# Kernel optimization log

Hardware: AMD Instinct MI355X
Metric: run time of the kernel (lower is better)

## Reference

```python
import jax, jax.numpy as jnp
import numpy as np

B, S, D_IN, D_OUT = 8, 2048, 512, 512


def setup_inputs() -> dict:
    key = jax.random.key(0)
    ks = jax.random.split(key, 6)
    return {
        "inputs_for_keys": jax.random.normal(ks[0], (B, S, D_IN), dtype=jnp.float32),
        "inputs_for_values": jax.random.normal(ks[1], (B, S, D_IN), dtype=jnp.float32),
        "inputs_for_queries": jax.random.normal(ks[2], (B, S, D_IN), dtype=jnp.float32),
        "Wq": jax.random.normal(ks[3], (D_IN, D_OUT), dtype=jnp.float32) * 0.05,
        "Wk": jax.random.normal(ks[4], (D_IN, D_OUT), dtype=jnp.float32) * 0.05,
        "Wv": jax.random.normal(ks[5], (D_IN, D_OUT), dtype=jnp.float32) * 0.05,
    }


def reference(inputs_for_keys, inputs_for_values, inputs_for_queries, Wq, Wk, Wv):
    # Projections: [B,S,D_in] @ [D_in,D_out] -> [B,S,D_out]
    Q = inputs_for_queries @ Wq
    K = inputs_for_keys @ Wk
    V = inputs_for_values @ Wv
    d_k = K.shape[-1]
    scale = 1.0 / jnp.sqrt(jnp.float32(d_k))
    # Scores: [B,Sq,Sk]
    scores = jnp.einsum("bqd,bkd->bqk", Q, K) * scale
    # Causal mask: original adds -inf for key positions j > query i (use_mask=True)
    q_idx = jnp.arange(Q.shape[1])[:, None]
    k_idx = jnp.arange(K.shape[1])[None, :]
    scores = jnp.where(k_idx > q_idx, jnp.float32(-jnp.inf), scores)
    attn = jax.nn.softmax(scores, axis=-1)
    return jnp.einsum("bqk,bkd->bqd", attn, V)
```

## Files before the change

kernel.cpp:

```cpp
#include <hip/hip_runtime.h>
#include <hip/hip_bf16.h>

typedef __bf16 bf16;
typedef __bf16 bf16x4 __attribute__((ext_vector_type(4)));
typedef __bf16 bf16x8 __attribute__((ext_vector_type(8)));
typedef float f32x4 __attribute__((ext_vector_type(4)));
typedef float f32x16 __attribute__((ext_vector_type(16)));

#define NB 8
#define NS 2048
#define ND 512

static __device__ __forceinline__ f32x4 mfma16(bf16x8 a, bf16x8 b, f32x4 c) {
  return __builtin_amdgcn_mfma_f32_16x16x32_bf16(a, b, c, 0, 0, 0);
}
static __device__ __forceinline__ f32x16 mfma32(bf16x8 a, bf16x8 b, f32x16 c) {
  return __builtin_amdgcn_mfma_f32_32x32x16_bf16(a, b, c, 0, 0, 0);
}
static __device__ __forceinline__ void async16(const bf16* g, bf16* l) {
  __builtin_amdgcn_global_load_lds((const __attribute__((address_space(1))) void*)g,
                                   (__attribute__((address_space(3))) void*)l, 16, 0, 0);
}

#define BAR_VM8_LG0() do { asm volatile("s_waitcnt vmcnt(8) lgkmcnt(0)" ::: "memory"); \
  __builtin_amdgcn_s_barrier(); __builtin_amdgcn_sched_barrier(0); } while (0)
#define BAR_LG0() do { asm volatile("s_waitcnt lgkmcnt(0)" ::: "memory"); \
  __builtin_amdgcn_s_barrier(); __builtin_amdgcn_sched_barrier(0); } while (0)

__global__ void wconv_kernel(const float* __restrict__ Wq,
                             const float* __restrict__ Wk,
                             const float* __restrict__ Wv,
                             bf16* __restrict__ Wt) {
  __shared__ float buf[64][65];
  const int z = blockIdx.z;
  const float* W = (z == 0) ? Wq : (z == 1) ? Wk : Wv;
  const float scale = (z == 0) ? 0.063763537f : 1.0f;
  const int k0 = blockIdx.x * 64, n0 = blockIdx.y * 64;
  const int t = threadIdx.x;
#pragma unroll
  for (int i = 0; i < 16; ++i) {
    int idx = i * 256 + t;
    int kk = idx >> 6, nn = idx & 63;
    buf[kk][nn] = W[(size_t)(k0 + kk) * 512 + n0 + nn];
  }
  __syncthreads();
#pragma unroll
  for (int i = 0; i < 16; ++i) {
    int idx = i * 256 + t;
    int nn = idx >> 6, kk = idx & 63;
    Wt[(size_t)z * 262144 + (size_t)(n0 + nn) * 512 + k0 + (kk ^ ((nn & 7) << 3))] =
        (bf16)(buf[kk][nn] * scale);
  }
}

__launch_bounds__(256)
__global__ void proj_kernel(const float* __restrict__ Xq,
                            const float* __restrict__ Xk,
                            const float* __restrict__ Xv,
                            const bf16* __restrict__ Wt,
                            bf16* __restrict__ Cq,
                            bf16* __restrict__ Ck,
                            bf16* __restrict__ Cv) {
  __shared__ bf16 As[2][128][72];
  __shared__ bf16 WsL[2][8192];
  const int z = blockIdx.z;
  const float* A = (z == 0) ? Xq : (z == 1) ? Xk : Xv;
  const bf16* Wz = Wt + (size_t)z * 262144;
  bf16* C = (z == 0) ? Cq : (z == 1) ? Ck : Cv;

  const int t = threadIdx.x;
  const int lane = t & 63;
  const int w = t >> 6;
  const int wr = w >> 1, wc = w & 1;
  const int bxr = blockIdx.x;
  const int mt = (bxr & 7) * 16 + (bxr >> 3);
  const int bm = mt * 128;
  const int bn = blockIdx.y * 128;

  f32x4 acc[4][4] = {};

  auto stageA = [&](int kc, int bufi) {
    int r0 = t >> 4, seg = t & 15;
#pragma unroll
    for (int p = 0; p < 8; ++p) {
      int r = p * 16 + r0;
      float4 v = *(const float4*)(A + (size_t)(bm + r) * 512 + kc * 64 + seg * 4);
      bf16x4 o = {(bf16)v.x, (bf16)v.y, (bf16)v.z, (bf16)v.w};
      *(bf16x4*)&As[bufi][r][seg * 4] = o;
    }
  };
  auto stageW = [&](int kc, int bufi) {
    const int n = t >> 3, seg = t & 7;
#pragma unroll
    for (int i = 0; i < 4; ++i)
      async16(Wz + (size_t)(bn + i * 32 + n) * 512 + kc * 64 + seg * 8,
              &WsL[bufi][(i * 32 + n) * 64 + seg * 8]);
  };

  stageW(0, 0);
  stageA(0, 0);
  __syncthreads();
  int buf = 0;
  for (int kc = 0; kc < 8; ++kc) {
    if (kc < 7) { stageW(kc + 1, buf ^ 1); stageA(kc + 1, buf ^ 1); }
    const int arow = lane & 15, kq = (lane >> 4) * 8;
#pragma unroll
    for (int kk = 0; kk < 2; ++kk) {
      bf16x8 af[4], bfr[4];
#pragma unroll
      for (int mi = 0; mi < 4; ++mi)
        af[mi] = *(const bf16x8*)&As[buf][wr * 64 + mi * 16 + arow][kk * 32 + kq];
#pragma unroll
      for (int ni = 0; ni < 4; ++ni) {
        int n = wc * 64 + ni * 16 + arow;
        bfr[ni] = *(const bf16x8*)&WsL[buf][n * 64 + ((kk * 32 + kq) ^ ((n & 7) << 3))];
      }
#pragma unroll
      for (int mi = 0; mi < 4; ++mi)
#pragma unroll
        for (int ni = 0; ni < 4; ++ni)
          acc[mi][ni] = mfma16(af[mi], bfr[ni], acc[mi][ni]);
    }
    __syncthreads();
    buf ^= 1;
  }

  const int row0 = (lane >> 4) * 4, col = lane & 15;
#pragma unroll
  for (int mi = 0; mi < 4; ++mi)
#pragma unroll
    for (int ni = 0; ni < 4; ++ni) {
      int cg = bn + wc * 64 + ni * 16 + col;
#pragma unroll
      for (int j = 0; j < 4; ++j) {
        int rg = bm + wr * 64 + mi * 16 + row0 + j;
        bf16 o = (bf16)acc[mi][ni][j];
        if (z == 0) {
          C[(size_t)rg * ND + cg] = o;
        } else if (z == 1) {
          C[(size_t)rg * ND + (cg ^ ((rg & 7) << 3))] = o;
        } else {
          int bb = rg >> 11, s = rg & 2047;
          int ss = (s & ~63) | ((s & 63) ^ ((cg & 7) << 3));
          C[(size_t)bb * (ND * NS) + (size_t)cg * NS + ss] = o;
        }
      }
    }
}

template<int NSPLIT>
__launch_bounds__(512, 2)
__global__ void attn_kernel(const bf16* __restrict__ Qg,
                            const bf16* __restrict__ Kg,
                            const bf16* __restrict__ Vtg,
                            float* __restrict__ Out,
                            bf16* __restrict__ Pn,
                            float* __restrict__ Mp,
                            float* __restrict__ Lp) {
  __shared__ bf16 Ks[64][512];
  __shared__ bf16 Vts[512][64];
  __shared__ float Ss[64][68];
  __shared__ bf16 Ps[64][72];
  __shared__ float m_lds[64], l_lds[64], r_lds[64];

  const int t = threadIdx.x;
  const int lane = t & 63;
  const int w = t >> 6;
  const int id = blockIdx.x;
  const int b = id & 7;
  const int qt = 31 - ((id >> 3) & 31);
  const int h = (NSPLIT == 2) ? (id >> 8) : 0;
  const int q0 = qt * 64;
  const int sm = w >> 2, sn = (w >> 1) & 1, sk = w & 1;
  const int l31 = lane & 31, lhi = lane >> 5;

  int t_begin, t_end;
  {
    int nt = qt + 1;
    int mid = (nt + 1) >> 1;
    if (NSPLIT == 2) { t_begin = h ? mid : 0; t_end = h ? nt : mid; }
    else { t_begin = 0; t_end = nt; }
  }
  const int pidx = (h * 8 + b) * 32 + qt;

  if (NSPLIT == 2 && t_begin >= t_end) {
    if (t < 64) { Mp[pidx * 64 + t] = -1e30f; Lp[pidx * 64 + t] = 0.0f; }
    return;
  }

  const bf16* Qb = Qg + (size_t)b * NS * ND;
  const bf16* Kb = Kg + (size_t)b * NS * ND;
  const bf16* Vb = Vtg + (size_t)b * ND * NS;

  if (t < 64) { m_lds[t] = -1e30f; l_lds[t] = 0.0f; }

  bf16x8 qf[16];
  {
    const bf16* qrow = Qb + (size_t)(q0 + sm * 32 + l31) * ND + sk * 256 + lhi * 8;
#pragma unroll
    for (int kc = 0; kc < 16; ++kc) qf[kc] = *(const bf16x8*)(qrow + kc * 16);
  }
  f32x16 acc[2][2] = {};

  auto stageK = [&](int k0s) {
#pragma unroll
    for (int i = 0; i < 8; ++i)
      async16(Kb + (size_t)(k0s + w * 8 + i) * ND + lane * 8, &Ks[w * 8 + i][0]);
  };
  auto stageV = [&](int k0s) {
#pragma unroll
    for (int i = 0; i < 8; ++i)
      async16(Vb + (size_t)(w * 64 + i * 8 + (lane >> 3)) * NS + k0s + (lane & 7) * 8,
              &Vts[w * 64 + i * 8][0]);
  };

  stageK(t_begin * 64);
  stageV(t_begin * 64);

  for (int it = t_begin; it < t_end; ++it) {
    const int k0 = it * 64;
    const int nx = (it + 1 < t_end ? it + 1 : it) * 64;
    BAR_VM8_LG0();

    __builtin_amdgcn_s_setprio(1);
    f32x16 sacc = {};
    const int kvr = sn * 32 + l31;
    const int swz = (kvr & 7) << 3;
#pragma unroll
    for (int kc = 0; kc < 16; ++kc) {
      int col = (sk * 256 + kc * 16 + lhi * 8) ^ swz;
      bf16x8 bfrag = *(const bf16x8*)&Ks[kvr][col];
      sacc = mfma32(qf[kc], bfrag, sacc);
    }
    __builtin_amdgcn_s_setprio(0);
    if (sk) {
#pragma unroll
      for (int j = 0; j < 16; ++j) {
        int row = (j & 3) + 8 * (j >> 2) + 4 * lhi;
        Ss[sm * 32 + row][sn * 32 + l31] = sacc[j];
      }
    }
    BAR_LG0();
    stageK(nx);
    if (!sk) {
      const bool mask = (it == qt);
#pragma unroll
      for (int j = 0; j < 16; ++j) {
        int row = (j & 3) + 8 * (j >> 2) + 4 * lhi;
        int q = sm * 32 + row, kvc = sn * 32 + l31;
        float v = sacc[j] + Ss[q][kvc];
        if (mask && (k0 + kvc > q0 + q)) v = -1e30f;
        Ss[q][kvc] = v;
      }
    }
    BAR_LG0();

    {
      const int row = t >> 3, sub = t & 7;
      float4 a = *(const float4*)&Ss[row][sub * 8];
      float4 c = *(const float4*)&Ss[row][sub * 8 + 4];
      float mx = fmaxf(fmaxf(fmaxf(a.x, a.y), fmaxf(a.z, a.w)),
                       fmaxf(fmaxf(c.x, c.y), fmaxf(c.z, c.w)));
#pragma unroll
      for (int d = 1; d < 8; d <<= 1) mx = fmaxf(mx, __shfl_xor(mx, d));
      float m_old = m_lds[row];
      float m_new = fmaxf(m_old, mx);
      float p0 = exp2f(a.x - m_new), p1 = exp2f(a.y - m_new);
      float p2 = exp2f(a.z - m_new), p3 = exp2f(a.w - m_new);
      float p4 = exp2f(c.x - m_new), p5 = exp2f(c.y - m_new);
      float p6 = exp2f(c.z - m_new), p7 = exp2f(c.w - m_new);
      float sum = ((p0 + p1) + (p2 + p3)) + ((p4 + p5) + (p6 + p7));
#pragma unroll
      for (int d = 1; d < 8; d <<= 1) sum += __shfl_xor(sum, d);
      bf16x8 pv = {(bf16)p0, (bf16)p1, (bf16)p2, (bf16)p3,
                   (bf16)p4, (bf16)p5, (bf16)p6, (bf16)p7};
      *(bf16x8*)&Ps[row][sub * 8] = pv;
      if (sub == 0) {
        float rs = exp2f(m_old - m_new);
        r_lds[row] = rs;
        m_lds[row] = m_new;
        l_lds[row] = l_lds[row] * rs + sum;
      }
    }
    BAR_VM8_LG0();

    __builtin_amdgcn_s_setprio(1);
#pragma unroll
    for (int mi = 0; mi < 2; ++mi)
#pragma unroll
      for (int j = 0; j < 16; ++j) {
        int row = mi * 32 + (j & 3) + 8 * (j >> 2) + 4 * lhi;
        float rs = r_lds[row];
        acc[mi][0][j] *= rs;
        acc[mi][1][j] *= rs;
      }
#pragma unroll
    for (int kc = 0; kc < 4; ++kc) {
      const int kv0 = kc * 16 + lhi * 8;
      bf16x8 pa0 = *(const bf16x8*)&Ps[l31][kv0];
      bf16x8 pa1 = *(const bf16x8*)&Ps[32 + l31][kv0];
      bf16x8 vb0, vb1;
      { int d0 = w * 64 + l31;      vb0 = *(const bf16x8*)&Vts[d0][kv0 ^ ((d0 & 7) << 3)]; }
      { int d1 = w * 64 + 32 + l31; vb1 = *(const bf16x8*)&Vts[d1][kv0 ^ ((d1 & 7) << 3)]; }
      acc[0][0] = mfma32(pa0, vb0, acc[0][0]);
      acc[0][1] = mfma32(pa0, vb1, acc[0][1]);
      acc[1][0] = mfma32(pa1, vb0, acc[1][0]);
      acc[1][1] = mfma32(pa1, vb1, acc[1][1]);
    }
    __builtin_amdgcn_s_setprio(0);
    BAR_LG0();
    stageV(nx);
  }

  if (NSPLIT == 2) {
    if (t < 64) { Mp[pidx * 64 + t] = m_lds[t]; Lp[pidx * 64 + t] = l_lds[t]; }
    bf16* Ob = Pn + (size_t)pidx * 64 * ND;
#pragma unroll
    for (int mi = 0; mi < 2; ++mi)
#pragma unroll
      for (int j = 0; j < 16; ++j) {
        int row = mi * 32 + (j & 3) + 8 * (j >> 2) + 4 * lhi;
        float inv = 1.0f / l_lds[row];
#pragma unroll
        for (int ni = 0; ni < 2; ++ni)
          Ob[(size_t)row * ND + w * 64 + ni * 32 + l31] = (bf16)(acc[mi][ni][j] * inv);
      }
  } else {
    float* Ob = Out + (size_t)b * NS * ND;
#pragma unroll
    for (int mi = 0; mi < 2; ++mi)
#pragma unroll
      for (int j = 0; j < 16; ++j) {
        int row = mi * 32 + (j & 3) + 8 * (j >> 2) + 4 * lhi;
        float inv = 1.0f / l_lds[row];
#pragma unroll
        for (int ni = 0; ni < 2; ++ni)
          __builtin_nontemporal_store(acc[mi][ni][j] * inv,
              &Ob[(size_t)(q0 + row) * ND + w * 64 + ni * 32 + l31]);
      }
  }
}

__global__ void combine_kernel(const bf16* __restrict__ Pn,
                               const float* __restrict__ Mp,
                               const float* __restrict__ Lp,
                               float* __restrict__ Out) {
  const int total = NB * NS * ND / 4;
  for (int v = blockIdx.x * 256 + threadIdx.x; v < total; v += gridDim.x * 256) {
    int e = v * 4;
    int d = e & 511;
    int s = (e >> 9) & 2047;
    int bb = e >> 20;
    int qt = s >> 6, r = s & 63;
    int p0 = (bb * 32 + qt) * 64 + r;
    int p1 = ((8 + bb) * 32 + qt) * 64 + r;
    float m0 = Mp[p0], l0 = Lp[p0], m1 = Mp[p1], l1 = Lp[p1];
    float M = fmaxf(m0, m1);
    float w0 = l0 * exp2f(m0 - M), w1 = l1 * exp2f(m1 - M);
    float inv = 1.0f / (w0 + w1);
    bf16x4 o0 = *(const bf16x4*)(Pn + (size_t)p0 * ND + d);
    bf16x4 o1 = *(const bf16x4*)(Pn + (size_t)p1 * ND + d);
    f32x4 o;
    o[0] = (w0 * (float)o0[0] + w1 * (float)o1[0]) * inv;
    o[1] = (w0 * (float)o0[1] + w1 * (float)o1[1]) * inv;
    o[2] = (w0 * (float)o0[2] + w1 * (float)o1[2]) * inv;
    o[3] = (w0 * (float)o0[3] + w1 * (float)o1[3]) * inv;
    __builtin_nontemporal_store(o, (f32x4*)(Out + e));
  }
}

extern "C" void kernel_launch(void* const* d_in, const int* in_sizes, int n_in,
                              void* d_out, int out_size, void* d_ws, size_t ws_size,
                              hipStream_t stream) {
  const float* Xk = (const float*)d_in[0];
  const float* Xv = (const float*)d_in[1];
  const float* Xq = (const float*)d_in[2];
  const float* Wq = (const float*)d_in[3];
  const float* Wk = (const float*)d_in[4];
  const float* Wv = (const float*)d_in[5];
  float* Out = (float*)d_out;

  char* ws = (char*)d_ws;
  bf16* Qb = (bf16*)(ws);
  bf16* Kb = (bf16*)(ws + (size_t)16 * 1024 * 1024);
  bf16* Vt = (bf16*)(ws + (size_t)32 * 1024 * 1024);
  bf16* Wt = (bf16*)(ws + (size_t)48 * 1024 * 1024);
  bf16* Pn = (bf16*)(ws + (size_t)50 * 1024 * 1024);
  float* Mp = (float*)(ws + (size_t)82 * 1024 * 1024);
  float* Lp = (float*)(ws + (size_t)82 * 1024 * 1024 + 131072);
  const bool split = ws_size >= (size_t)83 * 1024 * 1024;

  wconv_kernel<<<dim3(8, 8, 3), 256, 0, stream>>>(Wq, Wk, Wv, Wt);
  proj_kernel<<<dim3(128, 4, 3), 256, 0, stream>>>(Xq, Xk, Xv, Wt, Qb, Kb, Vt);
  if (split) {
    attn_kernel<2><<<512, 512, 0, stream>>>(Qb, Kb, Vt, Out, Pn, Mp, Lp);
    combine_kernel<<<2048, 256, 0, stream>>>(Pn, Mp, Lp, Out);
  } else {
    attn_kernel<1><<<256, 512, 0, stream>>>(Qb, Kb, Vt, Out, Pn, Mp, Lp);
  }
}
```

Before: 165.3 us.

## Load V fragments directly to registers and merge split-K score partials in softmax

V tiles are no longer staged through shared memory. Each wave loads its own transposed-V MFMA fragments straight from global memory into registers, prefetched one iteration ahead, and the V swizzle in the projection epilogue is dropped. Both split-K halves of QK^T now write their partial scores to separate LDS buffers, and the softmax pass sums them and applies the causal mask, which removes one barrier per iteration. This cuts LDS traffic and barriers but uses more registers and depends on global-load latency being hidden. The wait counts in BAR_VM8_LG0 were tuned for the old async staging and may no longer match.

```diff
diff --git a/kernel.cpp b/kernel.cpp
--- a/kernel.cpp
+++ b/kernel.cpp
@@ -141,8 +141,7 @@
           C[(size_t)rg * ND + (cg ^ ((rg & 7) << 3))] = o;
         } else {
           int bb = rg >> 11, s = rg & 2047;
-          int ss = (s & ~63) | ((s & 63) ^ ((cg & 7) << 3));
-          C[(size_t)bb * (ND * NS) + (size_t)cg * NS + ss] = o;
+          C[(size_t)bb * (ND * NS) + (size_t)cg * NS + s] = o;
         }
       }
     }
@@ -158,8 +157,7 @@
                             float* __restrict__ Mp,
                             float* __restrict__ Lp) {
   __shared__ bf16 Ks[64][512];
-  __shared__ bf16 Vts[512][64];
-  __shared__ float Ss[64][68];
+  __shared__ float Ss[2][64][68];
   __shared__ bf16 Ps[64][72];
   __shared__ float m_lds[64], l_lds[64], r_lds[64];
 
@@ -201,21 +199,25 @@
     for (int kc = 0; kc < 16; ++kc) qf[kc] = *(const bf16x8*)(qrow + kc * 16);
   }
   f32x16 acc[2][2] = {};
+  bf16x8 vr[8];
 
   auto stageK = [&](int k0s) {
 #pragma unroll
     for (int i = 0; i < 8; ++i)
       async16(Kb + (size_t)(k0s + w * 8 + i) * ND + lane * 8, &Ks[w * 8 + i][0]);
   };
-  auto stageV = [&](int k0s) {
-#pragma unroll
-    for (int i = 0; i < 8; ++i)
-      async16(Vb + (size_t)(w * 64 + i * 8 + (lane >> 3)) * NS + k0s + (lane & 7) * 8,
-              &Vts[w * 64 + i * 8][0]);
+  auto issueV = [&](int k0s) {
+#pragma unroll
+    for (int kc = 0; kc < 4; ++kc)
+#pragma unroll
+      for (int ni = 0; ni < 2; ++ni) {
+        int d = w * 64 + ni * 32 + l31;
+        vr[kc * 2 + ni] = *(const bf16x8*)(Vb + (size_t)d * NS + k0s + kc * 16 + lhi * 8);
+      }
   };
 
   stageK(t_begin * 64);
-  stageV(t_begin * 64);
+  issueV(t_begin * 64);
 
   for (int it = t_begin; it < t_end; ++it) {
     const int k0 = it * 64;
@@ -233,47 +235,42 @@
       sacc = mfma32(qf[kc], bfrag, sacc);
     }
     __builtin_amdgcn_s_setprio(0);
-    if (sk) {
-#pragma unroll
-      for (int j = 0; j < 16; ++j) {
-        int row = (j & 3) + 8 * (j >> 2) + 4 * lhi;
-        Ss[sm * 32 + row][sn * 32 + l31] = sacc[j];
-      }
+#pragma unroll
+    for (int j = 0; j < 16; ++j) {
+      int row = (j & 3) + 8 * (j >> 2) + 4 * lhi;
+      Ss[sk][sm * 32 + row][sn * 32 + l31] = sacc[j];
     }
     BAR_LG0();
     stageK(nx);
-    if (!sk) {
-      const bool mask = (it == qt);
-#pragma unroll
-      for (int j = 0; j < 16; ++j) {
-        int row = (j & 3) + 8 * (j >> 2) + 4 * lhi;
-        int q = sm * 32 + row, kvc = sn * 32 + l31;
-        float v = sacc[j] + Ss[q][kvc];
-        if (mask && (k0 + kvc > q0 + q)) v = -1e30f;
-        Ss[q][kvc] = v;
-      }
-    }
-    BAR_LG0();
 
     {
       const int row = t >> 3, sub = t & 7;
-      float4 a = *(const float4*)&Ss[row][sub * 8];
-      float4 c = *(const float4*)&Ss[row][sub * 8 + 4];
-      float mx = fmaxf(fmaxf(fmaxf(a.x, a.y), fmaxf(a.z, a.w)),
-                       fmaxf(fmaxf(c.x, c.y), fmaxf(c.z, c.w)));
+      float4 a0 = *(const float4*)&Ss[0][row][sub * 8];
+      float4 a1 = *(const float4*)&Ss[0][row][sub * 8 + 4];
+      float4 b0 = *(const float4*)&Ss[1][row][sub * 8];
+      float4 b1 = *(const float4*)&Ss[1][row][sub * 8 + 4];
+      float v[8];
+      v[0] = a0.x + b0.x; v[1] = a0.y + b0.y; v[2] = a0.z + b0.z; v[3] = a0.w + b0.w;
+      v[4] = a1.x + b1.x; v[5] = a1.y + b1.y; v[6] = a1.z + b1.z; v[7] = a1.w + b1.w;
+      if (it == qt) {
+#pragma unroll
+        for (int e = 0; e < 8; ++e)
+          if (k0 + sub * 8 + e > q0 + row) v[e] = -1e30f;
+      }
+      float mx = fmaxf(fmaxf(fmaxf(v[0], v[1]), fmaxf(v[2], v[3])),
+                       fmaxf(fmaxf(v[4], v[5]), fmaxf(v[6], v[7])));
 #pragma unroll
       for (int d = 1; d < 8; d <<= 1) mx = fmaxf(mx, __shfl_xor(mx, d));
       float m_old = m_lds[row];
       float m_new = fmaxf(m_old, mx);
-      float p0 = exp2f(a.x - m_new), p1 = exp2f(a.y - m_new);
-      float p2 = exp2f(a.z - m_new), p3 = exp2f(a.w - m_new);
-      float p4 = exp2f(c.x - m_new), p5 = exp2f(c.y - m_new);
-      float p6 = exp2f(c.z - m_new), p7 = exp2f(c.w - m_new);
-      float sum = ((p0 + p1) + (p2 + p3)) + ((p4 + p5) + (p6 + p7));
+      float p[8];
+#pragma unroll
+      for (int e = 0; e < 8; ++e) p[e] = exp2f(v[e] - m_new);
+      float sum = ((p[0] + p[1]) + (p[2] + p[3])) + ((p[4] + p[5]) + (p[6] + p[7]));
 #pragma unroll
       for (int d = 1; d < 8; d <<= 1) sum += __shfl_xor(sum, d);
-      bf16x8 pv = {(bf16)p0, (bf16)p1, (bf16)p2, (bf16)p3,
-                   (bf16)p4, (bf16)p5, (bf16)p6, (bf16)p7};
+      bf16x8 pv = {(bf16)p[0], (bf16)p[1], (bf16)p[2], (bf16)p[3],
+                   (bf16)p[4], (bf16)p[5], (bf16)p[6], (bf16)p[7]};
       *(bf16x8*)&Ps[row][sub * 8] = pv;
       if (sub == 0) {
         float rs = exp2f(m_old - m_new);
@@ -299,17 +296,13 @@
       const int kv0 = kc * 16 + lhi * 8;
       bf16x8 pa0 = *(const bf16x8*)&Ps[l31][kv0];
       bf16x8 pa1 = *(const bf16x8*)&Ps[32 + l31][kv0];
-      bf16x8 vb0, vb1;
-      { int d0 = w * 64 + l31;      vb0 = *(const bf16x8*)&Vts[d0][kv0 ^ ((d0 & 7) << 3)]; }
-      { int d1 = w * 64 + 32 + l31; vb1 = *(const bf16x8*)&Vts[d1][kv0 ^ ((d1 & 7) << 3)]; }
-      acc[0][0] = mfma32(pa0, vb0, acc[0][0]);
-      acc[0][1] = mfma32(pa0, vb1, acc[0][1]);
-      acc[1][0] = mfma32(pa1, vb0, acc[1][0]);
-      acc[1][1] = mfma32(pa1, vb1, acc[1][1]);
+      acc[0][0] = mfma32(pa0, vr[kc * 2 + 0], acc[0][0]);
+      acc[0][1] = mfma32(pa0, vr[kc * 2 + 1], acc[0][1]);
+      acc[1][0] = mfma32(pa1, vr[kc * 2 + 0], acc[1][0]);
+      acc[1][1] = mfma32(pa1, vr[kc * 2 + 1], acc[1][1]);
     }
     __builtin_amdgcn_s_setprio(0);
-    BAR_LG0();
-    stageV(nx);
+    issueV(nx);
   }
 
   if (NSPLIT == 2) {
```

Result: slower. 176.8 us (+7.0%).

## Restructure attention to 32-wide KV tiles, 256 threads, in-register softmax

Applied to the files above, without the earlier changes.

Rewrites the attention kernel to use 32-key tiles with 256-thread blocks. Each wave keeps its own running max and sum in registers, and the cross-wave score exchange goes through bf16 LDS instead of fp32. The KV split now divides each q-tile's 32-wide key tiles evenly between two blocks, which balances the causal work. The non-split fallback is removed and the V-transpose swizzle is changed to match the new 32-wide layout. The aim is less LDS traffic, fewer barriers and better balance. The trade-off is more iterations, a larger per-wave accumulator (8 f32x16) that raises register pressure, and reduced precision in the partial scores.

```diff
diff --git a/kernel.cpp b/kernel.cpp
--- a/kernel.cpp
+++ b/kernel.cpp
@@ -141,204 +141,183 @@
           C[(size_t)rg * ND + (cg ^ ((rg & 7) << 3))] = o;
         } else {
           int bb = rg >> 11, s = rg & 2047;
-          int ss = (s & ~63) | ((s & 63) ^ ((cg & 7) << 3));
+          int ss = (s & ~31) | ((((s >> 3) & 3) ^ ((cg ^ (cg >> 2)) & 3)) << 3) | (s & 7);
           C[(size_t)bb * (ND * NS) + (size_t)cg * NS + ss] = o;
         }
       }
     }
 }
 
-template<int NSPLIT>
-__launch_bounds__(512, 2)
+__launch_bounds__(256, 2)
 __global__ void attn_kernel(const bf16* __restrict__ Qg,
                             const bf16* __restrict__ Kg,
                             const bf16* __restrict__ Vtg,
-                            float* __restrict__ Out,
                             bf16* __restrict__ Pn,
                             float* __restrict__ Mp,
                             float* __restrict__ Lp) {
-  __shared__ bf16 Ks[64][512];
-  __shared__ bf16 Vts[512][64];
-  __shared__ float Ss[64][68];
-  __shared__ bf16 Ps[64][72];
-  __shared__ float m_lds[64], l_lds[64], r_lds[64];
+  __shared__ bf16 Ks[32 * 512];
+  __shared__ bf16 Vts[512 * 32];
+  __shared__ bf16 Sx[64 * 40];
+  __shared__ bf16 Ps[64 * 40];
+  __shared__ float r_lds[64], l_lds[64];
 
   const int t = threadIdx.x;
   const int lane = t & 63;
   const int w = t >> 6;
+  const int l31 = lane & 31, lhi = lane >> 5;
+  const int sq = w >> 1, sk = w & 1;
   const int id = blockIdx.x;
-  const int b = id & 7;
-  const int qt = 31 - ((id >> 3) & 31);
-  const int h = (NSPLIT == 2) ? (id >> 8) : 0;
+  int b, qt, h;
+  if (id < 256) { b = id & 7; qt = 31 - (id >> 3); h = 0; }
+  else { int j = id - 256; b = j & 7; qt = j >> 3; h = 1; }
   const int q0 = qt * 64;
-  const int sm = w >> 2, sn = (w >> 1) & 1, sk = w & 1;
-  const int l31 = lane & 31, lhi = lane >> 5;
-
-  int t_begin, t_end;
-  {
-    int nt = qt + 1;
-    int mid = (nt + 1) >> 1;
-    if (NSPLIT == 2) { t_begin = h ? mid : 0; t_end = h ? nt : mid; }
-    else { t_begin = 0; t_end = nt; }
-  }
+  const int t_begin = h ? (qt + 1) : 0;
+  const int t_end = h ? (2 * qt + 2) : (qt + 1);
   const int pidx = (h * 8 + b) * 32 + qt;
-
-  if (NSPLIT == 2 && t_begin >= t_end) {
-    if (t < 64) { Mp[pidx * 64 + t] = -1e30f; Lp[pidx * 64 + t] = 0.0f; }
-    return;
-  }
 
   const bf16* Qb = Qg + (size_t)b * NS * ND;
   const bf16* Kb = Kg + (size_t)b * NS * ND;
   const bf16* Vb = Vtg + (size_t)b * ND * NS;
 
-  if (t < 64) { m_lds[t] = -1e30f; l_lds[t] = 0.0f; }
+  const int qg = q0 + sq * 32 + l31;
+  const int qsw = (qg >> 3) & 3;
+  const int ql = sq * 32 + l31;
 
   bf16x8 qf[16];
   {
-    const bf16* qrow = Qb + (size_t)(q0 + sm * 32 + l31) * ND + sk * 256 + lhi * 8;
+    const bf16* qrow = Qb + (size_t)qg * ND + sk * 256 + lhi * 8;
 #pragma unroll
     for (int kc = 0; kc < 16; ++kc) qf[kc] = *(const bf16x8*)(qrow + kc * 16);
   }
-  f32x16 acc[2][2] = {};
+  f32x16 acc[8] = {};
+  float m_run = -1e30f, l_run = 0.0f;
 
   auto stageK = [&](int k0s) {
 #pragma unroll
     for (int i = 0; i < 8; ++i)
-      async16(Kb + (size_t)(k0s + w * 8 + i) * ND + lane * 8, &Ks[w * 8 + i][0]);
+      async16(Kb + (size_t)(k0s + w * 8 + i) * ND + lane * 8, &Ks[(w * 8 + i) * 512]);
   };
   auto stageV = [&](int k0s) {
 #pragma unroll
-    for (int i = 0; i < 8; ++i)
-      async16(Vb + (size_t)(w * 64 + i * 8 + (lane >> 3)) * NS + k0s + (lane & 7) * 8,
-              &Vts[w * 64 + i * 8][0]);
+    for (int i = 0; i < 8; ++i) {
+      int d = (w * 8 + i) * 16 + (lane >> 2);
+      async16(Vb + (size_t)d * NS + k0s + (lane & 3) * 8, &Vts[(w * 8 + i) * 512]);
+    }
   };
 
-  stageK(t_begin * 64);
-  stageV(t_begin * 64);
+  stageK(t_begin * 32);
+  stageV(t_begin * 32);
 
   for (int it = t_begin; it < t_end; ++it) {
-    const int k0 = it * 64;
-    const int nx = (it + 1 < t_end ? it + 1 : it) * 64;
+    const int k0 = it * 32;
+    const int nx = (it + 1 < t_end ? it + 1 : it) * 32;
     BAR_VM8_LG0();
 
     __builtin_amdgcn_s_setprio(1);
     f32x16 sacc = {};
-    const int kvr = sn * 32 + l31;
-    const int swz = (kvr & 7) << 3;
 #pragma unroll
     for (int kc = 0; kc < 16; ++kc) {
-      int col = (sk * 256 + kc * 16 + lhi * 8) ^ swz;
-      bf16x8 bfrag = *(const bf16x8*)&Ks[kvr][col];
-      sacc = mfma32(qf[kc], bfrag, sacc);
+      int col = (sk * 256 + kc * 16 + lhi * 8) ^ ((l31 & 7) << 3);
+      bf16x8 kf = *(const bf16x8*)&Ks[l31 * 512 + col];
+      sacc = mfma32(kf, qf[kc], sacc);
     }
     __builtin_amdgcn_s_setprio(0);
     if (sk) {
 #pragma unroll
-      for (int j = 0; j < 16; ++j) {
-        int row = (j & 3) + 8 * (j >> 2) + 4 * lhi;
-        Ss[sm * 32 + row][sn * 32 + l31] = sacc[j];
+      for (int jg = 0; jg < 4; ++jg) {
+        bf16x4 v = {(bf16)sacc[jg * 4], (bf16)sacc[jg * 4 + 1],
+                    (bf16)sacc[jg * 4 + 2], (bf16)sacc[jg * 4 + 3]};
+        *(bf16x4*)&Sx[ql * 40 + ((jg ^ qsw) << 3) + 4 * lhi] = v;
       }
     }
     BAR_LG0();
     stageK(nx);
+
     if (!sk) {
-      const bool mask = (it == qt);
-#pragma unroll
-      for (int j = 0; j < 16; ++j) {
-        int row = (j & 3) + 8 * (j >> 2) + 4 * lhi;
-        int q = sm * 32 + row, kvc = sn * 32 + l31;
-        float v = sacc[j] + Ss[q][kvc];
-        if (mask && (k0 + kvc > q0 + q)) v = -1e30f;
-        Ss[q][kvc] = v;
-      }
-    }
-    BAR_LG0();
-
-    {
-      const int row = t >> 3, sub = t & 7;
-      float4 a = *(const float4*)&Ss[row][sub * 8];
-      float4 c = *(const float4*)&Ss[row][sub * 8 + 4];
-      float mx = fmaxf(fmaxf(fmaxf(a.x, a.y), fmaxf(a.z, a.w)),
-                       fmaxf(fmaxf(c.x, c.y), fmaxf(c.z, c.w)));
-#pragma unroll
-      for (int d = 1; d < 8; d <<= 1) mx = fmaxf(mx, __shfl_xor(mx, d));
-      float m_old = m_lds[row];
-      float m_new = fmaxf(m_old, mx);
-      float p0 = exp2f(a.x - m_new), p1 = exp2f(a.y - m_new);
-      float p2 = exp2f(a.z - m_new), p3 = exp2f(a.w - m_new);
-      float p4 = exp2f(c.x - m_new), p5 = exp2f(c.y - m_new);
-      float p6 = exp2f(c.z - m_new), p7 = exp2f(c.w - m_new);
-      float sum = ((p0 + p1) + (p2 + p3)) + ((p4 + p5) + (p6 + p7));
-#pragma unroll
-      for (int d = 1; d < 8; d <<= 1) sum += __shfl_xor(sum, d);
-      bf16x8 pv = {(bf16)p0, (bf16)p1, (bf16)p2, (bf16)p3,
-                   (bf16)p4, (bf16)p5, (bf16)p6, (bf16)p7};
-      *(bf16x8*)&Ps[row][sub * 8] = pv;
-      if (sub == 0) {
-        float rs = exp2f(m_old - m_new);
-        r_lds[row] = rs;
-        m_lds[row] = m_new;
-        l_lds[row] = l_lds[row] * rs + sum;
+      float v[16];
+#pragma unroll
+      for (int jg = 0; jg < 4; ++jg) {
+        bf16x4 x = *(const bf16x4*)&Sx[ql * 40 + ((jg ^ qsw) << 3) + 4 * lhi];
+#pragma unroll
+        for (int e = 0; e < 4; ++e) v[jg * 4 + e] = sacc[jg * 4 + e] + (float)x[e];
+      }
+      if (k0 + 31 > q0) {
+#pragma unroll
+        for (int jg = 0; jg < 4; ++jg)
+#pragma unroll
+          for (int e = 0; e < 4; ++e)
+            if (k0 + jg * 8 + 4 * lhi + e > qg) v[jg * 4 + e] = -1e30f;
+      }
+      float mx = v[0];
+#pragma unroll
+      for (int j = 1; j < 16; ++j) mx = fmaxf(mx, v[j]);
+      mx = fmaxf(mx, __shfl_xor(mx, 32));
+      float mn = fmaxf(m_run, mx);
+      float rr = exp2f(m_run - mn);
+      float p[16], sum = 0.0f;
+#pragma unroll
+      for (int j = 0; j < 16; ++j) { p[j] = exp2f(v[j] - mn); sum += p[j]; }
+      sum += __shfl_xor(sum, 32);
+      m_run = mn;
+      l_run = l_run * rr + sum;
+      r_lds[ql] = rr;
+#pragma unroll
+      for (int jg = 0; jg < 4; ++jg) {
+        bf16x4 pv = {(bf16)p[jg * 4], (bf16)p[jg * 4 + 1],
+                     (bf16)p[jg * 4 + 2], (bf16)p[jg * 4 + 3]};
+        *(bf16x4*)&Ps[ql * 40 + ((jg ^ qsw) << 3) + 4 * lhi] = pv;
       }
     }
     BAR_VM8_LG0();
 
+    float rf[16];
+#pragma unroll
+    for (int j = 0; j < 16; ++j)
+      rf[j] = r_lds[sq * 32 + (j & 3) + 8 * (j >> 2) + 4 * lhi];
+#pragma unroll
+    for (int dt = 0; dt < 8; ++dt)
+#pragma unroll
+      for (int j = 0; j < 16; ++j) acc[dt][j] *= rf[j];
+    bf16x8 paf[2];
+#pragma unroll
+    for (int kc = 0; kc < 2; ++kc)
+      paf[kc] = *(const bf16x8*)&Ps[ql * 40 + (((kc * 2 + lhi) ^ qsw) << 3)];
     __builtin_amdgcn_s_setprio(1);
 #pragma unroll
-    for (int mi = 0; mi < 2; ++mi)
-#pragma unroll
-      for (int j = 0; j < 16; ++j) {
-        int row = mi * 32 + (j & 3) + 8 * (j >> 2) + 4 * lhi;
-        float rs = r_lds[row];
-        acc[mi][0][j] *= rs;
-        acc[mi][1][j] *= rs;
-      }
-#pragma unroll
-    for (int kc = 0; kc < 4; ++kc) {
-      const int kv0 = kc * 16 + lhi * 8;
-      bf16x8 pa0 = *(const bf16x8*)&Ps[l31][kv0];
-      bf16x8 pa1 = *(const bf16x8*)&Ps[32 + l31][kv0];
-      bf16x8 vb0, vb1;
-      { int d0 = w * 64 + l31;      vb0 = *(const bf16x8*)&Vts[d0][kv0 ^ ((d0 & 7) << 3)]; }
-      { int d1 = w * 64 + 32 + l31; vb1 = *(const bf16x8*)&Vts[d1][kv0 ^ ((d1 & 7) << 3)]; }
-      acc[0][0] = mfma32(pa0, vb0, acc[0][0]);
-      acc[0][1] = mfma32(pa0, vb1, acc[0][1]);
-      acc[1][0] = mfma32(pa1, vb0, acc[1][0]);
-      acc[1][1] = mfma32(pa1, vb1, acc[1][1]);
+    for (int dt = 0; dt < 8; ++dt) {
+      int d = sk * 256 + dt * 32 + l31;
+      int so = (d ^ (d >> 2)) & 3;
+#pragma unroll
+      for (int kc = 0; kc < 2; ++kc) {
+        bf16x8 vf = *(const bf16x8*)&Vts[d * 32 + (((kc * 2 + lhi) ^ so) << 3)];
+        acc[dt] = mfma32(paf[kc], vf, acc[dt]);
+      }
     }
     __builtin_amdgcn_s_setprio(0);
     BAR_LG0();
     stageV(nx);
   }
 
-  if (NSPLIT == 2) {
-    if (t < 64) { Mp[pidx * 64 + t] = m_lds[t]; Lp[pidx * 64 + t] = l_lds[t]; }
-    bf16* Ob = Pn + (size_t)pidx * 64 * ND;
-#pragma unroll
-    for (int mi = 0; mi < 2; ++mi)
-#pragma unroll
-      for (int j = 0; j < 16; ++j) {
-        int row = mi * 32 + (j & 3) + 8 * (j >> 2) + 4 * lhi;
-        float inv = 1.0f / l_lds[row];
-#pragma unroll
-        for (int ni = 0; ni < 2; ++ni)
-          Ob[(size_t)row * ND + w * 64 + ni * 32 + l31] = (bf16)(acc[mi][ni][j] * inv);
-      }
-  } else {
-    float* Ob = Out + (size_t)b * NS * ND;
-#pragma unroll
-    for (int mi = 0; mi < 2; ++mi)
-#pragma unroll
-      for (int j = 0; j < 16; ++j) {
-        int row = mi * 32 + (j & 3) + 8 * (j >> 2) + 4 * lhi;
-        float inv = 1.0f / l_lds[row];
-#pragma unroll
-        for (int ni = 0; ni < 2; ++ni)
-          __builtin_nontemporal_store(acc[mi][ni][j] * inv,
-              &Ob[(size_t)(q0 + row) * ND + w * 64 + ni * 32 + l31]);
-      }
-  }
+  if (!sk) {
+    l_lds[ql] = l_run;
+    Mp[pidx * 64 + ql] = m_run;
+    Lp[pidx * 64 + ql] = l_run;
+  }
+  __syncthreads();
+  float linv[16];
+#pragma unroll
+  for (int j = 0; j < 16; ++j) {
+    float lv = l_lds[sq * 32 + (j & 3) + 8 * (j >> 2) + 4 * lhi];
+    linv[j] = (lv > 0.0f) ? 1.0f / lv : 0.0f;
+  }
+  bf16* Ob = Pn + (size_t)pidx * 64 * ND;
+#pragma unroll
+  for (int dt = 0; dt < 8; ++dt)
+#pragma unroll
+    for (int j = 0; j < 16; ++j) {
+      int row = sq * 32 + (j & 3) + 8 * (j >> 2) + 4 * lhi;
+      Ob[(size_t)row * ND + sk * 256 + dt * 32 + l31] = (bf16)(acc[dt][j] * linv[j]);
+    }
 }
 
 __global__ void combine_kernel(const bf16* __restrict__ Pn,
@@ -388,14 +367,9 @@
   bf16* Pn = (bf16*)(ws + (size_t)50 * 1024 * 1024);
   float* Mp = (float*)(ws + (size_t)82 * 1024 * 1024);
   float* Lp = (float*)(ws + (size_t)82 * 1024 * 1024 + 131072);
-  const bool split = ws_size >= (size_t)83 * 1024 * 1024;
 
   wconv_kernel<<<dim3(8, 8, 3), 256, 0, stream>>>(Wq, Wk, Wv, Wt);
   proj_kernel<<<dim3(128, 4, 3), 256, 0, stream>>>(Xq, Xk, Xv, Wt, Qb, Kb, Vt);
-  if (split) {
-    attn_kernel<2><<<512, 512, 0, stream>>>(Qb, Kb, Vt, Out, Pn, Mp, Lp);
-    combine_kernel<<<2048, 256, 0, stream>>>(Pn, Mp, Lp, Out);
-  } else {
-    attn_kernel<1><<<256, 512, 0, stream>>>(Qb, Kb, Vt, Out, Pn, Mp, Lp);
-  }
-}
+  attn_kernel<<<512, 256, 0, stream>>>(Qb, Kb, Vt, Pn, Mp, Lp);
+  combine_kernel<<<2048, 256, 0, stream>>>(Pn, Mp, Lp, Out);
+}
```

Measured after the change: 242.9 us. 46.9% more time.

## Pair long and short causal split halves in one persistent attention block

Applied to the files above, without the earlier changes.

Replaces the 512-block split-KV launch with 256 blocks that each handle two phases: the first half of KV tiles for query tile 31-c, then the second half for query tile c. The pairing gives every block about the same amount of causal work, so the lopsided per-block work of the old launch no longer leaves some blocks idle while others finish. The cost is that each block's work is serialized, with a full barrier between phases and a pipeline refill per phase. The unsplit fallback path is removed, so the kernel now always needs the larger workspace and the combine kernel.

```diff
diff --git a/kernel.cpp b/kernel.cpp
--- a/kernel.cpp
+++ b/kernel.cpp
@@ -148,12 +148,10 @@
     }
 }
 
-template<int NSPLIT>
 __launch_bounds__(512, 2)
 __global__ void attn_kernel(const bf16* __restrict__ Qg,
                             const bf16* __restrict__ Kg,
                             const bf16* __restrict__ Vtg,
-                            float* __restrict__ Out,
                             bf16* __restrict__ Pn,
                             float* __restrict__ Mp,
                             float* __restrict__ Lp) {
@@ -168,39 +166,13 @@
   const int w = t >> 6;
   const int id = blockIdx.x;
   const int b = id & 7;
-  const int qt = 31 - ((id >> 3) & 31);
-  const int h = (NSPLIT == 2) ? (id >> 8) : 0;
-  const int q0 = qt * 64;
+  const int c = id >> 3;
   const int sm = w >> 2, sn = (w >> 1) & 1, sk = w & 1;
   const int l31 = lane & 31, lhi = lane >> 5;
-
-  int t_begin, t_end;
-  {
-    int nt = qt + 1;
-    int mid = (nt + 1) >> 1;
-    if (NSPLIT == 2) { t_begin = h ? mid : 0; t_end = h ? nt : mid; }
-    else { t_begin = 0; t_end = nt; }
-  }
-  const int pidx = (h * 8 + b) * 32 + qt;
-
-  if (NSPLIT == 2 && t_begin >= t_end) {
-    if (t < 64) { Mp[pidx * 64 + t] = -1e30f; Lp[pidx * 64 + t] = 0.0f; }
-    return;
-  }
 
   const bf16* Qb = Qg + (size_t)b * NS * ND;
   const bf16* Kb = Kg + (size_t)b * NS * ND;
   const bf16* Vb = Vtg + (size_t)b * ND * NS;
-
-  if (t < 64) { m_lds[t] = -1e30f; l_lds[t] = 0.0f; }
-
-  bf16x8 qf[16];
-  {
-    const bf16* qrow = Qb + (size_t)(q0 + sm * 32 + l31) * ND + sk * 256 + lhi * 8;
-#pragma unroll
-    for (int kc = 0; kc < 16; ++kc) qf[kc] = *(const bf16x8*)(qrow + kc * 16);
-  }
-  f32x16 acc[2][2] = {};
 
   auto stageK = [&](int k0s) {
 #pragma unroll
@@ -214,105 +186,132 @@
               &Vts[w * 64 + i * 8][0]);
   };
 
-  stageK(t_begin * 64);
-  stageV(t_begin * 64);
-
-  for (int it = t_begin; it < t_end; ++it) {
-    const int k0 = it * 64;
-    const int nx = (it + 1 < t_end ? it + 1 : it) * 64;
-    BAR_VM8_LG0();
-
-    __builtin_amdgcn_s_setprio(1);
-    f32x16 sacc = {};
-    const int kvr = sn * 32 + l31;
-    const int swz = (kvr & 7) << 3;
-#pragma unroll
-    for (int kc = 0; kc < 16; ++kc) {
-      int col = (sk * 256 + kc * 16 + lhi * 8) ^ swz;
-      bf16x8 bfrag = *(const bf16x8*)&Ks[kvr][col];
-      sacc = mfma32(qf[kc], bfrag, sacc);
-    }
-    __builtin_amdgcn_s_setprio(0);
-    if (sk) {
-#pragma unroll
-      for (int j = 0; j < 16; ++j) {
-        int row = (j & 3) + 8 * (j >> 2) + 4 * lhi;
-        Ss[sm * 32 + row][sn * 32 + l31] = sacc[j];
-      }
-    }
-    BAR_LG0();
-    stageK(nx);
-    if (!sk) {
-      const bool mask = (it == qt);
-#pragma unroll
-      for (int j = 0; j < 16; ++j) {
-        int row = (j & 3) + 8 * (j >> 2) + 4 * lhi;
-        int q = sm * 32 + row, kvc = sn * 32 + l31;
-        float v = sacc[j] + Ss[q][kvc];
-        if (mask && (k0 + kvc > q0 + q)) v = -1e30f;
-        Ss[q][kvc] = v;
-      }
-    }
-    BAR_LG0();
-
+  for (int phase = 0; phase < 2; ++phase) {
+    const int qt = phase ? c : (31 - c);
+    const int q0 = qt * 64;
+    const int nt = qt + 1;
+    const int mid = (nt + 1) >> 1;
+    const int t_begin = phase ? mid : 0;
+    const int t_end = phase ? nt : mid;
+    const int pidx = (phase * 8 + b) * 32 + qt;
+
+    if (phase) {
+      asm volatile("s_waitcnt vmcnt(0) lgkmcnt(0)" ::: "memory");
+      __builtin_amdgcn_s_barrier();
+      __builtin_amdgcn_sched_barrier(0);
+    }
+    if (t_begin >= t_end) {
+      if (t < 64) { Mp[pidx * 64 + t] = -1e30f; Lp[pidx * 64 + t] = 0.0f; }
+      continue;
+    }
+    if (t < 64) { m_lds[t] = -1e30f; l_lds[t] = 0.0f; }
+
+    bf16x8 qf[16];
     {
-      const int row = t >> 3, sub = t & 7;
-      float4 a = *(const float4*)&Ss[row][sub * 8];
-      float4 c = *(const float4*)&Ss[row][sub * 8 + 4];
-      float mx = fmaxf(fmaxf(fmaxf(a.x, a.y), fmaxf(a.z, a.w)),
-                       fmaxf(fmaxf(c.x, c.y), fmaxf(c.z, c.w)));
-#pragma unroll
-      for (int d = 1; d < 8; d <<= 1) mx = fmaxf(mx, __shfl_xor(mx, d));
-      float m_old = m_lds[row];
-      float m_new = fmaxf(m_old, mx);
-      float p0 = exp2f(a.x - m_new), p1 = exp2f(a.y - m_new);
-      float p2 = exp2f(a.z - m_new), p3 = exp2f(a.w - m_new);
-      float p4 = exp2f(c.x - m_new), p5 = exp2f(c.y - m_new);
-      float p6 = exp2f(c.z - m_new), p7 = exp2f(c.w - m_new);
-      float sum = ((p0 + p1) + (p2 + p3)) + ((p4 + p5) + (p6 + p7));
-#pragma unroll
-      for (int d = 1; d < 8; d <<= 1) sum += __shfl_xor(sum, d);
-      bf16x8 pv = {(bf16)p0, (bf16)p1, (bf16)p2, (bf16)p3,
-                   (bf16)p4, (bf16)p5, (bf16)p6, (bf16)p7};
-      *(bf16x8*)&Ps[row][sub * 8] = pv;
-      if (sub == 0) {
-        float rs = exp2f(m_old - m_new);
-        r_lds[row] = rs;
-        m_lds[row] = m_new;
-        l_lds[row] = l_lds[row] * rs + sum;
-      }
-    }
-    BAR_VM8_LG0();
-
-    __builtin_amdgcn_s_setprio(1);
-#pragma unroll
-    for (int mi = 0; mi < 2; ++mi)
-#pragma unroll
-      for (int j = 0; j < 16; ++j) {
-        int row = mi * 32 + (j & 3) + 8 * (j >> 2) + 4 * lhi;
-        float rs = r_lds[row];
-        acc[mi][0][j] *= rs;
-        acc[mi][1][j] *= rs;
-      }
-#pragma unroll
-    for (int kc = 0; kc < 4; ++kc) {
-      const int kv0 = kc * 16 + lhi * 8;
-      bf16x8 pa0 = *(const bf16x8*)&Ps[l31][kv0];
-      bf16x8 pa1 = *(const bf16x8*)&Ps[32 + l31][kv0];
-      bf16x8 vb0, vb1;
-      { int d0 = w * 64 + l31;      vb0 = *(const bf16x8*)&Vts[d0][kv0 ^ ((d0 & 7) << 3)]; }
-      { int d1 = w * 64 + 32 + l31; vb1 = *(const bf16x8*)&Vts[d1][kv0 ^ ((d1 & 7) << 3)]; }
-      acc[0][0] = mfma32(pa0, vb0, acc[0][0]);
-      acc[0][1] = mfma32(pa0, vb1, acc[0][1]);
-      acc[1][0] = mfma32(pa1, vb0, acc[1][0]);
-      acc[1][1] = mfma32(pa1, vb1, acc[1][1]);
-    }
-    __builtin_amdgcn_s_setprio(0);
-    BAR_LG0();
-    stageV(nx);
-  }
-
-  if (NSPLIT == 2) {
+      const bf16* qrow = Qb + (size_t)(q0 + sm * 32 + l31) * ND + sk * 256 + lhi * 8;
+#pragma unroll
+      for (int kc = 0; kc < 16; ++kc) qf[kc] = *(const bf16x8*)(qrow + kc * 16);
+    }
+    f32x16 acc[2][2] = {};
+
+    stageK(t_begin * 64);
+    stageV(t_begin * 64);
+
+    for (int it = t_begin; it < t_end; ++it) {
+      const int k0 = it * 64;
+      const int nx = (it + 1 < t_end ? it + 1 : it) * 64;
+      BAR_VM8_LG0();
+
+      __builtin_amdgcn_s_setprio(1);
+      f32x16 sacc = {};
+      const int kvr = sn * 32 + l31;
+      const int swz = (kvr & 7) << 3;
+#pragma unroll
+      for (int kc = 0; kc < 16; ++kc) {
+        int col = (sk * 256 + kc * 16 + lhi * 8) ^ swz;
+        bf16x8 bfrag = *(const bf16x8*)&Ks[kvr][col];
+        sacc = mfma32(qf[kc], bfrag, sacc);
+      }
+      __builtin_amdgcn_s_setprio(0);
+      if (sk) {
+#pragma unroll
+        for (int j = 0; j < 16; ++j) {
+          int row = (j & 3) + 8 * (j >> 2) + 4 * lhi;
+          Ss[sm * 32 + row][sn * 32 + l31] = sacc[j];
+        }
+      }
+      BAR_LG0();
+      stageK(nx);
+      if (!sk) {
+        const bool mask = (it == qt);
+#pragma unroll
+        for (int j = 0; j < 16; ++j) {
+          int row = (j & 3) + 8 * (j >> 2) + 4 * lhi;
+          int q = sm * 32 + row, kvc = sn * 32 + l31;
+          float v = sacc[j] + Ss[q][kvc];
+          if (mask && (k0 + kvc > q0 + q)) v = -1e30f;
+          Ss[q][kvc] = v;
+        }
+      }
+      BAR_LG0();
+
+      {
+        const int row = t >> 3, sub = t & 7;
+        float4 a = *(const float4*)&Ss[row][sub * 8];
+        float4 cc = *(const float4*)&Ss[row][sub * 8 + 4];
+        float mx = fmaxf(fmaxf(fmaxf(a.x, a.y), fmaxf(a.z, a.w)),
+                         fmaxf(fmaxf(cc.x, cc.y), fmaxf(cc.z, cc.w)));
+#pragma unroll
+        for (int d = 1; d < 8; d <<= 1) mx = fmaxf(mx, __shfl_xor(mx, d));
+        float m_old = m_lds[row];
+        float m_new = fmaxf(m_old, mx);
+        float p0 = exp2f(a.x - m_new), p1 = exp2f(a.y - m_new);
+        float p2 = exp2f(a.z - m_new), p3 = exp2f(a.w - m_new);
+        float p4 = exp2f(cc.x - m_new), p5 = exp2f(cc.y - m_new);
+        float p6 = exp2f(cc.z - m_new), p7 = exp2f(cc.w - m_new);
+        float sum = ((p0 + p1) + (p2 + p3)) + ((p4 + p5) + (p6 + p7));
+#pragma unroll
+        for (int d = 1; d < 8; d <<= 1) sum += __shfl_xor(sum, d);
+        bf16x8 pv = {(bf16)p0, (bf16)p1, (bf16)p2, (bf16)p3,
+                     (bf16)p4, (bf16)p5, (bf16)p6, (bf16)p7};
+        *(bf16x8*)&Ps[row][sub * 8] = pv;
+        if (sub == 0) {
+          float rs = exp2f(m_old - m_new);
+          r_lds[row] = rs;
+          m_lds[row] = m_new;
+          l_lds[row] = l_lds[row] * rs + sum;
+        }
+      }
+      BAR_VM8_LG0();
+
+      __builtin_amdgcn_s_setprio(1);
+#pragma unroll
+      for (int mi = 0; mi < 2; ++mi)
+#pragma unroll
+        for (int j = 0; j < 16; ++j) {
+          int row = mi * 32 + (j & 3) + 8 * (j >> 2) + 4 * lhi;
+          float rs = r_lds[row];
+          acc[mi][0][j] *= rs;
+          acc[mi][1][j] *= rs;
+        }
+#pragma unroll
+      for (int kc = 0; kc < 4; ++kc) {
+        const int kv0 = kc * 16 + lhi * 8;
+        bf16x8 pa0 = *(const bf16x8*)&Ps[l31][kv0];
+        bf16x8 pa1 = *(const bf16x8*)&Ps[32 + l31][kv0];
+        bf16x8 vb0, vb1;
+        { int d0 = w * 64 + l31;      vb0 = *(const bf16x8*)&Vts[d0][kv0 ^ ((d0 & 7) << 3)]; }
+        { int d1 = w * 64 + 32 + l31; vb1 = *(const bf16x8*)&Vts[d1][kv0 ^ ((d1 & 7) << 3)]; }
+        acc[0][0] = mfma32(pa0, vb0, acc[0][0]);
+        acc[0][1] = mfma32(pa0, vb1, acc[0][1]);
+        acc[1][0] = mfma32(pa1, vb0, acc[1][0]);
+        acc[1][1] = mfma32(pa1, vb1, acc[1][1]);
+      }
+      __builtin_amdgcn_s_setprio(0);
+      BAR_LG0();
+      stageV(nx);
+    }
+
     if (t < 64) { Mp[pidx * 64 + t] = m_lds[t]; Lp[pidx * 64 + t] = l_lds[t]; }
     bf16* Ob = Pn + (size_t)pidx * 64 * ND;
 #pragma unroll
@@ -324,19 +323,6 @@
 #pragma unroll
         for (int ni = 0; ni < 2; ++ni)
           Ob[(size_t)row * ND + w * 64 + ni * 32 + l31] = (bf16)(acc[mi][ni][j] * inv);
-      }
-  } else {
-    float* Ob = Out + (size_t)b * NS * ND;
-#pragma unroll
-    for (int mi = 0; mi < 2; ++mi)
-#pragma unroll
-      for (int j = 0; j < 16; ++j) {
-        int row = mi * 32 + (j & 3) + 8 * (j >> 2) + 4 * lhi;
-        float inv = 1.0f / l_lds[row];
-#pragma unroll
-        for (int ni = 0; ni < 2; ++ni)
-          __builtin_nontemporal_store(acc[mi][ni][j] * inv,
-              &Ob[(size_t)(q0 + row) * ND + w * 64 + ni * 32 + l31]);
       }
   }
 }
@@ -388,14 +374,9 @@
   bf16* Pn = (bf16*)(ws + (size_t)50 * 1024 * 1024);
   float* Mp = (float*)(ws + (size_t)82 * 1024 * 1024);
   float* Lp = (float*)(ws + (size_t)82 * 1024 * 1024 + 131072);
-  const bool split = ws_size >= (size_t)83 * 1024 * 1024;
 
   wconv_kernel<<<dim3(8, 8, 3), 256, 0, stream>>>(Wq, Wk, Wv, Wt);
   proj_kernel<<<dim3(128, 4, 3), 256, 0, stream>>>(Xq, Xk, Xv, Wt, Qb, Kb, Vt);
-  if (split) {
-    attn_kernel<2><<<512, 512, 0, stream>>>(Qb, Kb, Vt, Out, Pn, Mp, Lp);
-    combine_kernel<<<2048, 256, 0, stream>>>(Pn, Mp, Lp, Out);
-  } else {
-    attn_kernel<1><<<256, 512, 0, stream>>>(Qb, Kb, Vt, Out, Pn, Mp, Lp);
-  }
-}
+  attn_kernel<<<256, 512, 0, stream>>>(Qb, Kb, Vt, Pn, Mp, Lp);
+  combine_kernel<<<2048, 256, 0, stream>>>(Pn, Mp, Lp, Out);
+}
```

Measured after the change: 183.5 us. 1.11x slower.
